# Performance work log

Measured on AMD Instinct MI355X. Metric: run time of the kernel, lower is better.

The kernel has to match this reference:

```python
import jax, jax.numpy as jnp
import numpy as np

HEAD_N = 16
EMBED_D = 1024
MASK_FILL = 1e-09  # source uses masked_fill(mask==0, 1e-09), NOT -inf


def setup_inputs() -> dict:
    key = jax.random.key(0)
    ks = jax.random.split(key, 8)
    B, S, D = 4, 4096, EMBED_D
    L = S // HEAD_N
    q = jax.random.normal(ks[0], (B, S, D), dtype=jnp.float32)
    k = jax.random.normal(ks[1], (B, S, D), dtype=jnp.float32)
    v = jax.random.normal(ks[2], (B, S, D), dtype=jnp.float32)
    mask = jax.random.randint(ks[3], (B, L, L), 0, 2, dtype=jnp.int32)
    scale = 0.02
    Wq = jax.random.normal(ks[4], (D, D), dtype=jnp.float32) * scale
    Wk = jax.random.normal(ks[5], (D, D), dtype=jnp.float32) * scale
    Wv = jax.random.normal(ks[6], (D, D), dtype=jnp.float32) * scale
    Wo = jax.random.normal(ks[7], (D, D), dtype=jnp.float32) * scale
    return {"q": q, "k": k, "v": v, "mask": mask, "Wq": Wq, "Wk": Wk, "Wv": Wv, "Wo": Wo}


def _split_heads(x, B):
    # Faithful to source bug: view(B, -1, head_n, embedding_d).transpose(1, 2)
    # -> splits the SEQUENCE dim by head_n; per-head dim stays EMBED_D.
    return x.reshape(B, -1, HEAD_N, EMBED_D).transpose(0, 2, 1, 3)  # [B,h,L,D]


def reference(q, k, v, mask, Wq, Wk, Wv, Wo):
    B, S, D = q.shape
    qh = _split_heads(q @ Wq, B)
    kh = _split_heads(k @ Wk, B)
    vh = _split_heads(v @ Wv, B)
    # score: [B, h, L, L], L = S // head_n
    score = jnp.einsum("bhld,bhmd->bhlm", qh, kh) / jnp.sqrt(jnp.float32(D))
    m = mask[:, None, :, :]  # unsqueeze(1) -> broadcast over heads
    score = jnp.where(m == 0, jnp.float32(MASK_FILL), score)
    att = jax.nn.softmax(score, axis=-1)  # dropout p=0.0 -> identity
    x = jnp.einsum("bhlm,bhmd->bhld", att, vh)  # [B,h,L,D]
    x = x.transpose(0, 2, 1, 3).reshape(B, S, D)
    return x @ Wo
```

## Files before the change

kernel.cpp:

```cpp
#include <hip/hip_runtime.h>
#include <hip/hip_bf16.h>

typedef __bf16 bf16x8 __attribute__((ext_vector_type(8)));
typedef float f32x4 __attribute__((ext_vector_type(4)));
typedef unsigned short ushort_t;
typedef unsigned int uint_t;

#define HN 16
#define LSEQ 256
#define DD 1024
#define BB 4
#define SS 4096
#define MROWS (BB * SS)
#define BHN (BB * HN)

__device__ __forceinline__ ushort_t f2bf(float f) {
  uint_t u = __builtin_bit_cast(uint_t, f);
  u += 0x7fffu + ((u >> 16) & 1u);
  return (ushort_t)(u >> 16);
}
__device__ __forceinline__ uint_t pk2(float lo, float hi) {
  return (uint_t)f2bf(lo) | ((uint_t)f2bf(hi) << 16);
}

__global__ __launch_bounds__(256) void cvt_bf16(const float4* __restrict__ in,
                                                uint4* __restrict__ out) {
  const long i = (long)blockIdx.x * 256 + threadIdx.x;
  const float4 a = in[i * 2];
  const float4 b = in[i * 2 + 1];
  uint4 o;
  o.x = pk2(a.x, a.y);
  o.y = pk2(a.z, a.w);
  o.z = pk2(b.x, b.y);
  o.w = pk2(b.z, b.w);
  out[i] = o;
}

__global__ __launch_bounds__(256) void transpose_w(const float* __restrict__ W,
                                                   ushort_t* __restrict__ WT) {
  __shared__ float tile[32][33];
  const int tx = threadIdx.x, ty = threadIdx.y;
  const int bn = blockIdx.x * 32, bk = blockIdx.y * 32;
#pragma unroll
  for (int j = 0; j < 32; j += 8)
    tile[ty + j][tx] = W[(long)(bk + ty + j) * DD + bn + tx];
  __syncthreads();
#pragma unroll
  for (int j = 0; j < 32; j += 8)
    WT[(long)(bn + ty + j) * DD + bk + tx] = f2bf(tile[tx][ty + j]);
}

__global__ __launch_bounds__(256) void transpose_v(const ushort_t* __restrict__ vh,
                                                   ushort_t* __restrict__ vhT) {
  __shared__ ushort_t tile[32][33];
  const int tx = threadIdx.x, ty = threadIdx.y;
  const long zo = (long)blockIdx.z * (LSEQ * DD);
  const ushort_t* src = vh + zo;
  ushort_t* dst = vhT + zo;
  const int bd = blockIdx.x * 32;
  const int bl = blockIdx.y * 32;
#pragma unroll
  for (int j = 0; j < 32; j += 8)
    tile[ty + j][tx] = src[(long)(bl + ty + j) * DD + bd + tx];
  __syncthreads();
#pragma unroll
  for (int j = 0; j < 32; j += 8)
    dst[(long)(bd + ty + j) * LSEQ + bl + tx] = tile[tx][ty + j];
}

__global__ __launch_bounds__(256) void softmax_mask(const float* __restrict__ Sc,
                                                    const int* __restrict__ mask,
                                                    ushort_t* __restrict__ att) {
  const int wid = threadIdx.x >> 6, lane = threadIdx.x & 63;
  const int g = blockIdx.x * 4 + wid;
  const int bh = g >> 8, l = g & 255;
  const int b = bh >> 4;
  const float4 sv = *(const float4*)&Sc[(long)g * 256 + lane * 4];
  const int4 mv = *(const int4*)&mask[((long)b * 256 + l) * 256 + lane * 4];
  float s[4];
  s[0] = (mv.x == 0) ? 1e-9f : sv.x * 0.03125f;
  s[1] = (mv.y == 0) ? 1e-9f : sv.y * 0.03125f;
  s[2] = (mv.z == 0) ? 1e-9f : sv.z * 0.03125f;
  s[3] = (mv.w == 0) ? 1e-9f : sv.w * 0.03125f;
  float mx = fmaxf(fmaxf(s[0], s[1]), fmaxf(s[2], s[3]));
#pragma unroll
  for (int off = 32; off; off >>= 1) mx = fmaxf(mx, __shfl_xor(mx, off));
  float e[4], sum = 0.f;
#pragma unroll
  for (int i = 0; i < 4; ++i) {
    e[i] = __expf(s[i] - mx);
    sum += e[i];
  }
#pragma unroll
  for (int off = 32; off; off >>= 1) sum += __shfl_xor(sum, off);
  const float inv = 1.0f / sum;
  ushort4 o;
  o.x = f2bf(e[0] * inv);
  o.y = f2bf(e[1] * inv);
  o.z = f2bf(e[2] * inv);
  o.w = f2bf(e[3] * inv);
  *(ushort4*)&att[(long)g * 256 + lane * 4] = o;
}

template <int SMODE>
__global__ __launch_bounds__(256, 2) void gemm_tn(const ushort_t* __restrict__ Ab,
                                                  const ushort_t* __restrict__ Btp,
                                                  void* __restrict__ Cp, int K, int ldA,
                                                  int ldB, int ldC, long batchA,
                                                  long batchB, long batchC) {
  __shared__ ushort_t smem[16384];
  ushort_t* sA = smem;
  ushort_t* sB = smem + 8192;

  const int bx = blockIdx.x, by = blockIdx.y, z = blockIdx.z;
  const int rowBase = by * 128;
  const int colBase = bx * 128;

  const int t = threadIdx.x;
  const int lane = t & 63;
  const int wid = t >> 6;
  const int wr = (wid >> 1) * 64;
  const int wc = (wid & 1) * 64;
  const int fr = lane & 15;
  const int fk = (lane >> 4) * 8;

  const ushort_t* Atile = Ab + batchA * z + (long)rowBase * ldA;
  const ushort_t* Btile = Btp + batchB * z + (long)colBase * ldB;

  f32x4 acc[4][4];
#pragma unroll
  for (int m = 0; m < 4; ++m)
#pragma unroll
    for (int n = 0; n < 4; ++n) acc[m][n] = (f32x4){0.f, 0.f, 0.f, 0.f};

  const int NT = K >> 5;

  auto stageAB = [&](int buf, int kt) {
    const long ko = (long)kt * 32;
#pragma unroll
    for (int i = 0; i < 2; ++i) {
      const int c = i * 256 + t;
      const int cw = i * 256 + (t & 192);
      __builtin_amdgcn_global_load_lds(
          (const __attribute__((address_space(1))) void*)(Atile + (long)(c >> 2) * ldA + ko +
                                                          (c & 3) * 8),
          (__attribute__((address_space(3))) void*)(sA + buf * 4096 + cw * 8), 16, 0, 0);
      __builtin_amdgcn_global_load_lds(
          (const __attribute__((address_space(1))) void*)(Btile + (long)(c >> 2) * ldB + ko +
                                                          (c & 3) * 8),
          (__attribute__((address_space(3))) void*)(sB + buf * 4096 + cw * 8), 16, 0, 0);
    }
  };

  stageAB(0, 0);
  __syncthreads();

  int cur = 0;
  for (int kt = 0; kt < NT; ++kt) {
    if (kt + 1 < NT) stageAB(cur ^ 1, kt + 1);

    bf16x8 af[4], bfv[4];
    const ushort_t* baseA = sA + cur * 4096 + fk;
    const ushort_t* baseB = sB + cur * 4096 + fk;
#pragma unroll
    for (int m = 0; m < 4; ++m) af[m] = *(const bf16x8*)(baseA + (wr + m * 16 + fr) * 32);
#pragma unroll
    for (int n = 0; n < 4; ++n) bfv[n] = *(const bf16x8*)(baseB + (wc + n * 16 + fr) * 32);

#pragma unroll
    for (int m = 0; m < 4; ++m)
#pragma unroll
      for (int n = 0; n < 4; ++n)
        acc[m][n] = __builtin_amdgcn_mfma_f32_16x16x32_bf16(af[m], bfv[n], acc[m][n], 0, 0, 0);

    __syncthreads();
    cur ^= 1;
  }

  const int rq = (lane >> 4) * 4;
  if constexpr (SMODE == 0) {
    float* Cf = (float*)Cp + batchC * z;
#pragma unroll
    for (int m = 0; m < 4; ++m)
#pragma unroll
      for (int n = 0; n < 4; ++n)
#pragma unroll
        for (int r = 0; r < 4; ++r)
          Cf[(long)(rowBase + wr + m * 16 + rq + r) * ldC + colBase + wc + n * 16 + fr] =
              acc[m][n][r];
  } else {
#pragma unroll
    for (int m = 0; m < 4; ++m)
#pragma unroll
      for (int n = 0; n < 4; ++n)
#pragma unroll
        for (int r = 0; r < 4; ++r)
          smem[(wr + m * 16 + rq + r) * 128 + wc + n * 16 + fr] = f2bf(acc[m][n][r]);
    __syncthreads();
    ushort_t* Cb = (ushort_t*)Cp;
    const int c8 = (lane & 15) * 8;
#pragma unroll
    for (int i = 0; i < 8; ++i) {
      const int row = i * 16 + wid * 4 + (lane >> 4);
      const uint4 val = *(const uint4*)(smem + row * 128 + c8);
      const int l = rowBase + row;
      const int orow = ((z >> 4) << 12) + l * 16 + (z & 15);
      *(uint4*)(Cb + (long)orow * 1024 + colBase + c8) = val;
    }
  }
}

#define SBAR() asm volatile("s_barrier" ::: "memory")
#define LGKM0() asm volatile("s_waitcnt lgkmcnt(0)" ::: "memory")
#define VMW2() asm volatile("s_waitcnt vmcnt(2)" ::: "memory")
#define VMW0() asm volatile("s_waitcnt vmcnt(0)" ::: "memory")

template <int SMODE>
__global__ __launch_bounds__(512, 1) void gemm256(const ushort_t* __restrict__ Ab,
                                                  const ushort_t* __restrict__ Btp,
                                                  void* __restrict__ Cp, int K, int ldA,
                                                  int ldB, int ldC, int nbx) {
  __shared__ ushort_t sm[65536];

  const int orig = blockIdx.x;
  const int cpx = (int)gridDim.x >> 3;
  const int wgid = (orig & 7) * cpx + (orig >> 3);
  const int by = wgid / nbx, bx = wgid % nbx;
  const int rowBase = by * 256, colBase = bx * 256;

  const int t = threadIdx.x;
  const int lane = t & 63;
  const int wid = t >> 6;
  const int wm = wid >> 2;
  const int wn = wid & 3;
  const int fr = lane & 15;
  const int q = lane >> 4;

  const int sw0 = ((q ^ (fr & 7)) * 8);
  const int sw1 = (((4 + q) ^ (fr & 7)) * 8);
  const int aoff0 = fr * 64 + sw0;
  const int aoff1 = fr * 64 + sw1;
  const int bbase = ((wn & 1) * 64 + fr) * 64;
  const int boff0 = bbase + sw0;
  const int boff1 = bbase + sw1;

  const ushort_t* srcA[2][2];
  const ushort_t* srcB[2][2];
  int ldsoff[2];
#pragma unroll
  for (int i = 0; i < 2; ++i) {
    const int c = i * 512 + t;
    const int rowc = c >> 3;
    const int gc = (c & 7) ^ (rowc & 7);
    srcA[0][i] = Ab + (long)(rowBase + rowc) * ldA + gc * 8;
    srcA[1][i] = Ab + (long)(rowBase + 128 + rowc) * ldA + gc * 8;
    srcB[0][i] = Btp + (long)(colBase + rowc) * ldB + gc * 8;
    srcB[1][i] = Btp + (long)(colBase + 128 + rowc) * ldB + gc * 8;
    ldsoff[i] = (c & ~63) * 8;
  }

#define STAGE(kind, h, T)                                                                   \
  do {                                                                                      \
    ushort_t* _d = sm + ((kind) ? 32768 : 0) + ((T) & 1) * 16384 + (h) * 8192;              \
    const ushort_t* _s0 = ((kind) ? srcB[h][0] : srcA[h][0]) + (long)(T) * 64;              \
    __builtin_amdgcn_global_load_lds((const __attribute__((address_space(1))) void*)_s0,    \
                                     (__attribute__((address_space(3))) void*)(_d + ldsoff[0]), \
                                     16, 0, 0);                                             \
    const ushort_t* _s1 = ((kind) ? srcB[h][1] : srcA[h][1]) + (long)(T) * 64;              \
    __builtin_amdgcn_global_load_lds((const __attribute__((address_space(1))) void*)_s1,    \
                                     (__attribute__((address_space(3))) void*)(_d + ldsoff[1]), \
                                     16, 0, 0);                                             \
  } while (0)

  f32x4 acc[8][4];
#pragma unroll
  for (int m = 0; m < 8; ++m)
#pragma unroll
    for (int n = 0; n < 4; ++n) acc[m][n] = (f32x4){0.f, 0.f, 0.f, 0.f};

  bf16x8 af[4][2], bf0[2][2], bf1[2][2];

#define LDA4(dbuf, msub)                                                         \
  do {                                                                           \
    const ushort_t* _b = sm + (dbuf)*16384 + wm * 8192 + (msub)*4096;            \
    _Pragma("unroll") for (int m2 = 0; m2 < 4; ++m2) {                           \
      af[m2][0] = *(const bf16x8*)(_b + m2 * 1024 + aoff0);                      \
      af[m2][1] = *(const bf16x8*)(_b + m2 * 1024 + aoff1);                      \
    }                                                                            \
  } while (0)

#define LDB2(dbuf, nsub, bfv)                                                    \
  do {                                                                           \
    const ushort_t* _b = sm + 32768 + (dbuf)*16384 + (wn >> 1) * 8192 + (nsub)*2048; \
    _Pragma("unroll") for (int n2 = 0; n2 < 2; ++n2) {                           \
      bfv[n2][0] = *(const bf16x8*)(_b + n2 * 1024 + boff0);                     \
      bfv[n2][1] = *(const bf16x8*)(_b + n2 * 1024 + boff1);                     \
    }                                                                            \
  } while (0)

#define MMQ(msub, nsub, bfv)                                                     \
  do {                                                                           \
    _Pragma("unroll") for (int m2 = 0; m2 < 4; ++m2)                             \
        _Pragma("unroll") for (int n2 = 0; n2 < 2; ++n2) {                       \
      acc[(msub)*4 + m2][(nsub)*2 + n2] = __builtin_amdgcn_mfma_f32_16x16x32_bf16( \
          af[m2][0], bfv[n2][0], acc[(msub)*4 + m2][(nsub)*2 + n2], 0, 0, 0);    \
      acc[(msub)*4 + m2][(nsub)*2 + n2] = __builtin_amdgcn_mfma_f32_16x16x32_bf16( \
          af[m2][1], bfv[n2][1], acc[(msub)*4 + m2][(nsub)*2 + n2], 0, 0, 0);    \
    }                                                                            \
  } while (0)

#define PH_OPEN() SBAR(); LGKM0(); __builtin_amdgcn_s_setprio(1)
#define PH_CLOSE() __builtin_amdgcn_s_setprio(0); SBAR()

  const int NT = K >> 6;
  const int NI = NT >> 1;

  STAGE(0, 0, 0);
  STAGE(0, 1, 0);
  STAGE(1, 0, 0);
  STAGE(1, 1, 0);
  STAGE(0, 0, 1);
  VMW2();
  SBAR();

  for (int it = 0; it < NI - 1; ++it) {
    const int T0 = 2 * it;
    LDA4(0, 0);
    LDB2(0, 0, bf0);
    STAGE(0, 1, T0 + 1);
    PH_OPEN(); MMQ(0, 0, bf0); PH_CLOSE();
    LDB2(0, 1, bf1);
    STAGE(1, 0, T0 + 1);
    PH_OPEN(); MMQ(0, 1, bf1); PH_CLOSE();
    LDA4(0, 1);
    STAGE(1, 1, T0 + 1);
    PH_OPEN(); MMQ(1, 1, bf1); PH_CLOSE();
    STAGE(0, 0, T0 + 2);
    SBAR();
    __builtin_amdgcn_s_setprio(1);
    MMQ(1, 0, bf0);
    __builtin_amdgcn_s_setprio(0);
    VMW2();
    SBAR();
    LDA4(1, 0);
    LDB2(1, 0, bf0);
    STAGE(0, 1, T0 + 2);
    PH_OPEN(); MMQ(0, 0, bf0); PH_CLOSE();
    LDB2(1, 1, bf1);
    STAGE(1, 0, T0 + 2);
    PH_OPEN(); MMQ(0, 1, bf1); PH_CLOSE();
    LDA4(1, 1);
    STAGE(1, 1, T0 + 2);
    PH_OPEN(); MMQ(1, 1, bf1); PH_CLOSE();
    STAGE(0, 0, T0 + 3);
    SBAR();
    __builtin_amdgcn_s_setprio(1);
    MMQ(1, 0, bf0);
    __builtin_amdgcn_s_setprio(0);
    VMW2();
    SBAR();
  }

  {
    LDA4(0, 0);
    LDB2(0, 0, bf0);
    STAGE(0, 1, NT - 1);
    PH_OPEN(); MMQ(0, 0, bf0); PH_CLOSE();
    LDB2(0, 1, bf1);
    STAGE(1, 0, NT - 1);
    PH_OPEN(); MMQ(0, 1, bf1); PH_CLOSE();
    LDA4(0, 1);
    STAGE(1, 1, NT - 1);
    PH_OPEN(); MMQ(1, 1, bf1); PH_CLOSE();
    SBAR();
    __builtin_amdgcn_s_setprio(1);
    MMQ(1, 0, bf0);
    __builtin_amdgcn_s_setprio(0);
    VMW0();
    SBAR();
    LDA4(1, 0);
    LDB2(1, 0, bf0);
    PH_OPEN(); MMQ(0, 0, bf0); PH_CLOSE();
    LDB2(1, 1, bf1);
    PH_OPEN(); MMQ(0, 1, bf1); PH_CLOSE();
    LDA4(1, 1);
    PH_OPEN(); MMQ(1, 1, bf1); PH_CLOSE();
    SBAR();
    MMQ(1, 0, bf0);
    SBAR();
  }

  const int rq = q * 4;
  if constexpr (SMODE == 0) {
    float* Cf = (float*)Cp;
#pragma unroll
    for (int m = 0; m < 8; ++m)
#pragma unroll
      for (int n = 0; n < 4; ++n)
#pragma unroll
        for (int r = 0; r < 4; ++r) {
          const int row = rowBase + wm * 128 + m * 16 + rq + r;
          const int col = colBase + wn * 64 + n * 16 + fr;
          Cf[(long)row * ldC + col] = acc[m][n][r];
        }
  } else {
#pragma unroll
    for (int m = 0; m < 8; ++m)
#pragma unroll
      for (int n = 0; n < 4; ++n)
#pragma unroll
        for (int r = 0; r < 4; ++r) {
          const int row = wm * 128 + m * 16 + rq + r;
          const int col = wn * 64 + n * 16 + fr;
          sm[row * 256 + (((col >> 3) ^ (row & 7)) * 8) + (col & 7)] = f2bf(acc[m][n][r]);
        }
    __syncthreads();
    ushort_t* Cb = (ushort_t*)Cp;
    const int cc = t & 31;
    const int r0 = t >> 5;
#pragma unroll
    for (int i = 0; i < 16; ++i) {
      const int row = r0 + i * 16;
      const uint4 val = *(const uint4*)(sm + row * 256 + ((cc ^ (row & 7)) * 8));
      const int grow = rowBase + row;
      const int b = grow >> 12;
      const int s = grow & 4095;
      const int orow = ((b << 4) + (s & 15)) * 256 + (s >> 4);
      *(uint4*)(Cb + (long)orow * 1024 + colBase + cc * 8) = val;
    }
  }
#undef STAGE
#undef LDA4
#undef LDB2
#undef MMQ
#undef PH_OPEN
#undef PH_CLOSE
}

extern "C" void kernel_launch(void* const* d_in, const int* in_sizes, int n_in,
                              void* d_out, int out_size, void* d_ws, size_t ws_size,
                              hipStream_t stream) {
  const float* q = (const float*)d_in[0];
  const float* k = (const float*)d_in[1];
  const float* v = (const float*)d_in[2];
  const int* mask = (const int*)d_in[3];
  const float* Wq = (const float*)d_in[4];
  const float* Wk = (const float*)d_in[5];
  const float* Wv = (const float*)d_in[6];
  const float* Wo = (const float*)d_in[7];
  float* out = (float*)d_out;

  char* ws = (char*)d_ws;
  const size_t MB = 1024 * 1024;
  ushort_t* WTq = (ushort_t*)(ws + 0 * MB);
  ushort_t* WTk = (ushort_t*)(ws + 2 * MB);
  ushort_t* WTv = (ushort_t*)(ws + 4 * MB);
  ushort_t* WTo = (ushort_t*)(ws + 6 * MB);
  ushort_t* buf0 = (ushort_t*)(ws + 8 * MB);
  ushort_t* qh = (ushort_t*)(ws + 40 * MB);
  ushort_t* kh = (ushort_t*)(ws + 72 * MB);
  ushort_t* vh = (ushort_t*)(ws + 104 * MB);
  ushort_t* vhT = (ushort_t*)(ws + 136 * MB);
  float* Sc = (float*)buf0;
  ushort_t* att = qh;
  ushort_t* x = kh;

  const dim3 tb(32, 8);
  transpose_w<<<dim3(32, 32), tb, 0, stream>>>(Wq, WTq);
  transpose_w<<<dim3(32, 32), tb, 0, stream>>>(Wk, WTk);
  transpose_w<<<dim3(32, 32), tb, 0, stream>>>(Wv, WTv);
  transpose_w<<<dim3(32, 32), tb, 0, stream>>>(Wo, WTo);

  cvt_bf16<<<8192, 256, 0, stream>>>((const float4*)q, (uint4*)buf0);
  gemm256<1><<<256, 512, 0, stream>>>(buf0, WTq, qh, 1024, 1024, 1024, 1024, 4);
  cvt_bf16<<<8192, 256, 0, stream>>>((const float4*)k, (uint4*)buf0);
  gemm256<1><<<256, 512, 0, stream>>>(buf0, WTk, kh, 1024, 1024, 1024, 1024, 4);
  cvt_bf16<<<8192, 256, 0, stream>>>((const float4*)v, (uint4*)buf0);
  gemm256<1><<<256, 512, 0, stream>>>(buf0, WTv, vh, 1024, 1024, 1024, 1024, 4);

  transpose_v<<<dim3(32, 8, BHN), tb, 0, stream>>>(vh, vhT);

  gemm_tn<0><<<dim3(2, 2, BHN), 256, 0, stream>>>(qh, kh, Sc, 1024, 1024, 1024, 256,
                                                  (long)256 * 1024, (long)256 * 1024,
                                                  (long)65536);
  softmax_mask<<<4096, 256, 0, stream>>>(Sc, mask, att);

  gemm_tn<2><<<dim3(8, 2, BHN), 256, 0, stream>>>(att, vhT, x, 256, 256, 256, 1024,
                                                  (long)65536, (long)262144, 0);

  gemm256<0><<<256, 512, 0, stream>>>(x, WTo, out, 1024, 1024, 1024, 1024, 4);
}
```

Before: 292.1 us.

## Fuse QK^T scores with masked softmax and batch QKV projections into one launch

Adds a score_sm kernel that computes the Q·K^T tile for 64 query rows in LDS, then applies the mask and softmax in place. This removes the fp32 score round-trip through global memory and the separate softmax launch. When the workspace is large enough, the three input conversions and three projection GEMMs are also merged into one launch each, over a z dimension, which should give better occupancy (768 blocks). The four weight transposes are merged into one launch too. The fused score kernel uses 80KB of LDS and only 256 blocks, which may cost occupancy.

```diff
diff --git a/kernel.cpp b/kernel.cpp
--- a/kernel.cpp
+++ b/kernel.cpp
@@ -23,8 +23,12 @@
   return (uint_t)f2bf(lo) | ((uint_t)f2bf(hi) << 16);
 }
 
-__global__ __launch_bounds__(256) void cvt_bf16(const float4* __restrict__ in,
-                                                uint4* __restrict__ out) {
+__global__ __launch_bounds__(256) void cvt3(const float4* __restrict__ s0,
+                                            const float4* __restrict__ s1,
+                                            const float4* __restrict__ s2,
+                                            uint4* __restrict__ out) {
+  const int z = blockIdx.y;
+  const float4* in = (z == 0) ? s0 : (z == 1) ? s1 : s2;
   const long i = (long)blockIdx.x * 256 + threadIdx.x;
   const float4 a = in[i * 2];
   const float4 b = in[i * 2 + 1];
@@ -33,12 +37,18 @@
   o.y = pk2(a.z, a.w);
   o.z = pk2(b.x, b.y);
   o.w = pk2(b.z, b.w);
-  out[i] = o;
-}
-
-__global__ __launch_bounds__(256) void transpose_w(const float* __restrict__ W,
-                                                   ushort_t* __restrict__ WT) {
+  out[(long)z * 2097152 + i] = o;
+}
+
+__global__ __launch_bounds__(256) void transpose_w4(const float* __restrict__ W0,
+                                                    const float* __restrict__ W1,
+                                                    const float* __restrict__ W2,
+                                                    const float* __restrict__ W3,
+                                                    ushort_t* __restrict__ WT) {
   __shared__ float tile[32][33];
+  const int z = blockIdx.z;
+  const float* W = (z == 0) ? W0 : (z == 1) ? W1 : (z == 2) ? W2 : W3;
+  ushort_t* dst = WT + (long)z * 1048576;
   const int tx = threadIdx.x, ty = threadIdx.y;
   const int bn = blockIdx.x * 32, bk = blockIdx.y * 32;
 #pragma unroll
@@ -47,7 +57,7 @@
   __syncthreads();
 #pragma unroll
   for (int j = 0; j < 32; j += 8)
-    WT[(long)(bn + ty + j) * DD + bk + tx] = f2bf(tile[tx][ty + j]);
+    dst[(long)(bn + ty + j) * DD + bk + tx] = f2bf(tile[tx][ty + j]);
 }
 
 __global__ __launch_bounds__(256) void transpose_v(const ushort_t* __restrict__ vh,
@@ -68,38 +78,130 @@
     dst[(long)(bd + ty + j) * LSEQ + bl + tx] = tile[tx][ty + j];
 }
 
-__global__ __launch_bounds__(256) void softmax_mask(const float* __restrict__ Sc,
-                                                    const int* __restrict__ mask,
-                                                    ushort_t* __restrict__ att) {
-  const int wid = threadIdx.x >> 6, lane = threadIdx.x & 63;
-  const int g = blockIdx.x * 4 + wid;
-  const int bh = g >> 8, l = g & 255;
+__global__ __launch_bounds__(256, 2) void score_sm(const ushort_t* __restrict__ qh,
+                                                   const ushort_t* __restrict__ kh,
+                                                   const int* __restrict__ mask,
+                                                   ushort_t* __restrict__ att) {
+  __shared__ char smemraw[81920];
+  ushort_t* sA = (ushort_t*)smemraw;
+  ushort_t* sB = (ushort_t*)(smemraw + 16384);
+  float* Sf = (float*)smemraw;
+
+  const int orig = blockIdx.x;
+  const int wgid = (orig & 7) * 32 + (orig >> 3);
+  const int bh = wgid >> 2, rb = wgid & 3;
   const int b = bh >> 4;
-  const float4 sv = *(const float4*)&Sc[(long)g * 256 + lane * 4];
-  const int4 mv = *(const int4*)&mask[((long)b * 256 + l) * 256 + lane * 4];
-  float s[4];
-  s[0] = (mv.x == 0) ? 1e-9f : sv.x * 0.03125f;
-  s[1] = (mv.y == 0) ? 1e-9f : sv.y * 0.03125f;
-  s[2] = (mv.z == 0) ? 1e-9f : sv.z * 0.03125f;
-  s[3] = (mv.w == 0) ? 1e-9f : sv.w * 0.03125f;
-  float mx = fmaxf(fmaxf(s[0], s[1]), fmaxf(s[2], s[3]));
-#pragma unroll
-  for (int off = 32; off; off >>= 1) mx = fmaxf(mx, __shfl_xor(mx, off));
-  float e[4], sum = 0.f;
-#pragma unroll
-  for (int i = 0; i < 4; ++i) {
-    e[i] = __expf(s[i] - mx);
-    sum += e[i];
-  }
-#pragma unroll
-  for (int off = 32; off; off >>= 1) sum += __shfl_xor(sum, off);
-  const float inv = 1.0f / sum;
-  ushort4 o;
-  o.x = f2bf(e[0] * inv);
-  o.y = f2bf(e[1] * inv);
-  o.z = f2bf(e[2] * inv);
-  o.w = f2bf(e[3] * inv);
-  *(ushort4*)&att[(long)g * 256 + lane * 4] = o;
+  const ushort_t* A = qh + ((long)bh * 256 + rb * 64) * 1024;
+  const ushort_t* Bk = kh + (long)bh * 256 * 1024;
+
+  const int t = threadIdx.x, lane = t & 63, wid = t >> 6;
+  const int fr = lane & 15, q = lane >> 4;
+  const int wc = wid * 64;
+  const int sw0 = (q ^ (fr & 7)) * 8;
+  const int sw1 = ((4 + q) ^ (fr & 7)) * 8;
+
+  int srcAo[2], dstA[2], srcBo[8], dstB[8];
+#pragma unroll
+  for (int i = 0; i < 2; ++i) {
+    const int c = i * 256 + t, row = c >> 3, gc = (c & 7) ^ (row & 7);
+    srcAo[i] = row * 1024 + gc * 8;
+    dstA[i] = (i * 256 + (t & 192)) * 8;
+  }
+#pragma unroll
+  for (int i = 0; i < 8; ++i) {
+    const int c = i * 256 + t, row = c >> 3, gc = (c & 7) ^ (row & 7);
+    srcBo[i] = row * 1024 + gc * 8;
+    dstB[i] = (i * 256 + (t & 192)) * 8;
+  }
+
+  auto stage = [&](int buf, int kt) {
+    const int ko = kt * 64;
+#pragma unroll
+    for (int i = 0; i < 2; ++i)
+      __builtin_amdgcn_global_load_lds(
+          (const __attribute__((address_space(1))) void*)(A + srcAo[i] + ko),
+          (__attribute__((address_space(3))) void*)(sA + buf * 4096 + dstA[i]), 16, 0, 0);
+#pragma unroll
+    for (int i = 0; i < 8; ++i)
+      __builtin_amdgcn_global_load_lds(
+          (const __attribute__((address_space(1))) void*)(Bk + srcBo[i] + ko),
+          (__attribute__((address_space(3))) void*)(sB + buf * 16384 + dstB[i]), 16, 0, 0);
+  };
+
+  f32x4 acc[4][4];
+#pragma unroll
+  for (int m = 0; m < 4; ++m)
+#pragma unroll
+    for (int n = 0; n < 4; ++n) acc[m][n] = (f32x4){0.f, 0.f, 0.f, 0.f};
+
+  stage(0, 0);
+  __syncthreads();
+  int cur = 0;
+  for (int kt = 0; kt < 16; ++kt) {
+    if (kt < 15) stage(cur ^ 1, kt + 1);
+    bf16x8 af[4][2], bfv[4][2];
+    const ushort_t* bA = sA + cur * 4096;
+    const ushort_t* bB = sB + cur * 16384;
+#pragma unroll
+    for (int m = 0; m < 4; ++m) {
+      af[m][0] = *(const bf16x8*)(bA + (m * 16 + fr) * 64 + sw0);
+      af[m][1] = *(const bf16x8*)(bA + (m * 16 + fr) * 64 + sw1);
+    }
+#pragma unroll
+    for (int n = 0; n < 4; ++n) {
+      bfv[n][0] = *(const bf16x8*)(bB + (wc + n * 16 + fr) * 64 + sw0);
+      bfv[n][1] = *(const bf16x8*)(bB + (wc + n * 16 + fr) * 64 + sw1);
+    }
+#pragma unroll
+    for (int m = 0; m < 4; ++m)
+#pragma unroll
+      for (int n = 0; n < 4; ++n) {
+        acc[m][n] = __builtin_amdgcn_mfma_f32_16x16x32_bf16(af[m][0], bfv[n][0], acc[m][n], 0, 0, 0);
+        acc[m][n] = __builtin_amdgcn_mfma_f32_16x16x32_bf16(af[m][1], bfv[n][1], acc[m][n], 0, 0, 0);
+      }
+    __syncthreads();
+    cur ^= 1;
+  }
+
+#pragma unroll
+  for (int m = 0; m < 4; ++m)
+#pragma unroll
+    for (int n = 0; n < 4; ++n)
+#pragma unroll
+      for (int r = 0; r < 4; ++r)
+        Sf[(m * 16 + q * 4 + r) * 256 + wc + n * 16 + fr] = acc[m][n][r];
+  __syncthreads();
+
+#pragma unroll 2
+  for (int i = 0; i < 16; ++i) {
+    const int row = wid * 16 + i;
+    const int gl = rb * 64 + row;
+    const f32x4 sv = *(const f32x4*)&Sf[row * 256 + lane * 4];
+    const int4 mv = *(const int4*)&mask[((long)b * 256 + gl) * 256 + lane * 4];
+    float s[4];
+    s[0] = (mv.x == 0) ? 1e-9f : sv[0] * 0.03125f;
+    s[1] = (mv.y == 0) ? 1e-9f : sv[1] * 0.03125f;
+    s[2] = (mv.z == 0) ? 1e-9f : sv[2] * 0.03125f;
+    s[3] = (mv.w == 0) ? 1e-9f : sv[3] * 0.03125f;
+    float mx = fmaxf(fmaxf(s[0], s[1]), fmaxf(s[2], s[3]));
+#pragma unroll
+    for (int off = 32; off; off >>= 1) mx = fmaxf(mx, __shfl_xor(mx, off));
+    float e[4], sum = 0.f;
+#pragma unroll
+    for (int j = 0; j < 4; ++j) {
+      e[j] = __expf(s[j] - mx);
+      sum += e[j];
+    }
+#pragma unroll
+    for (int off = 32; off; off >>= 1) sum += __shfl_xor(sum, off);
+    const float inv = 1.0f / sum;
+    ushort4 o;
+    o.x = f2bf(e[0] * inv);
+    o.y = f2bf(e[1] * inv);
+    o.z = f2bf(e[2] * inv);
+    o.w = f2bf(e[3] * inv);
+    *(ushort4*)&att[((long)bh * 256 + gl) * 256 + lane * 4] = o;
+  }
 }
 
 template <int SMODE>
@@ -178,17 +280,7 @@
   }
 
   const int rq = (lane >> 4) * 4;
-  if constexpr (SMODE == 0) {
-    float* Cf = (float*)Cp + batchC * z;
-#pragma unroll
-    for (int m = 0; m < 4; ++m)
-#pragma unroll
-      for (int n = 0; n < 4; ++n)
-#pragma unroll
-        for (int r = 0; r < 4; ++r)
-          Cf[(long)(rowBase + wr + m * 16 + rq + r) * ldC + colBase + wc + n * 16 + fr] =
-              acc[m][n][r];
-  } else {
+  {
 #pragma unroll
     for (int m = 0; m < 4; ++m)
 #pragma unroll
@@ -216,17 +308,24 @@
 #define VMW0() asm volatile("s_waitcnt vmcnt(0)" ::: "memory")
 
 template <int SMODE>
-__global__ __launch_bounds__(512, 1) void gemm256(const ushort_t* __restrict__ Ab,
+__global__ __launch_bounds__(512, 1) void gemm256(const ushort_t* __restrict__ A0,
+                                                  const ushort_t* __restrict__ A1,
+                                                  const ushort_t* __restrict__ A2,
                                                   const ushort_t* __restrict__ Btp,
-                                                  void* __restrict__ Cp, int K, int ldA,
-                                                  int ldB, int ldC, int nbx) {
+                                                  void* __restrict__ Cp, long bStrideZ,
+                                                  long cStrideZ) {
   __shared__ ushort_t sm[65536];
 
   const int orig = blockIdx.x;
   const int cpx = (int)gridDim.x >> 3;
   const int wgid = (orig & 7) * cpx + (orig >> 3);
-  const int by = wgid / nbx, bx = wgid % nbx;
+  const int z = wgid >> 8;
+  const int tile = wgid & 255;
+  const int by = tile >> 2, bx = tile & 3;
   const int rowBase = by * 256, colBase = bx * 256;
+
+  const ushort_t* Ab = (z == 0) ? A0 : (z == 1) ? A1 : A2;
+  const ushort_t* Bt = Btp + bStrideZ * z;
 
   const int t = threadIdx.x;
   const int lane = t & 63;
@@ -252,10 +351,10 @@
     const int c = i * 512 + t;
     const int rowc = c >> 3;
     const int gc = (c & 7) ^ (rowc & 7);
-    srcA[0][i] = Ab + (long)(rowBase + rowc) * ldA + gc * 8;
-    srcA[1][i] = Ab + (long)(rowBase + 128 + rowc) * ldA + gc * 8;
-    srcB[0][i] = Btp + (long)(colBase + rowc) * ldB + gc * 8;
-    srcB[1][i] = Btp + (long)(colBase + 128 + rowc) * ldB + gc * 8;
+    srcA[0][i] = Ab + (long)(rowBase + rowc) * 1024 + gc * 8;
+    srcA[1][i] = Ab + (long)(rowBase + 128 + rowc) * 1024 + gc * 8;
+    srcB[0][i] = Bt + (long)(colBase + rowc) * 1024 + gc * 8;
+    srcB[1][i] = Bt + (long)(colBase + 128 + rowc) * 1024 + gc * 8;
     ldsoff[i] = (c & ~63) * 8;
   }
 
@@ -312,8 +411,8 @@
 #define PH_OPEN() SBAR(); LGKM0(); __builtin_amdgcn_s_setprio(1)
 #define PH_CLOSE() __builtin_amdgcn_s_setprio(0); SBAR()
 
-  const int NT = K >> 6;
-  const int NI = NT >> 1;
+  const int NT = 16;
+  const int NI = 8;
 
   STAGE(0, 0, 0);
   STAGE(0, 1, 0);
@@ -392,7 +491,7 @@
 
   const int rq = q * 4;
   if constexpr (SMODE == 0) {
-    float* Cf = (float*)Cp;
+    float* Cf = (float*)Cp + cStrideZ * z;
 #pragma unroll
     for (int m = 0; m < 8; ++m)
 #pragma unroll
@@ -401,7 +500,7 @@
         for (int r = 0; r < 4; ++r) {
           const int row = rowBase + wm * 128 + m * 16 + rq + r;
           const int col = colBase + wn * 64 + n * 16 + fr;
-          Cf[(long)row * ldC + col] = acc[m][n][r];
+          Cf[(long)row * 1024 + col] = acc[m][n][r];
         }
   } else {
 #pragma unroll
@@ -415,7 +514,7 @@
           sm[row * 256 + (((col >> 3) ^ (row & 7)) * 8) + (col & 7)] = f2bf(acc[m][n][r]);
         }
     __syncthreads();
-    ushort_t* Cb = (ushort_t*)Cp;
+    ushort_t* Cb = (ushort_t*)Cp + cStrideZ * z;
     const int cc = t & 31;
     const int r0 = t >> 5;
 #pragma unroll
@@ -452,41 +551,53 @@
 
   char* ws = (char*)d_ws;
   const size_t MB = 1024 * 1024;
-  ushort_t* WTq = (ushort_t*)(ws + 0 * MB);
-  ushort_t* WTk = (ushort_t*)(ws + 2 * MB);
-  ushort_t* WTv = (ushort_t*)(ws + 4 * MB);
-  ushort_t* WTo = (ushort_t*)(ws + 6 * MB);
-  ushort_t* buf0 = (ushort_t*)(ws + 8 * MB);
-  ushort_t* qh = (ushort_t*)(ws + 40 * MB);
-  ushort_t* kh = (ushort_t*)(ws + 72 * MB);
-  ushort_t* vh = (ushort_t*)(ws + 104 * MB);
-  ushort_t* vhT = (ushort_t*)(ws + 136 * MB);
-  float* Sc = (float*)buf0;
-  ushort_t* att = qh;
-  ushort_t* x = kh;
-
+  ushort_t* WT = (ushort_t*)ws;
   const dim3 tb(32, 8);
-  transpose_w<<<dim3(32, 32), tb, 0, stream>>>(Wq, WTq);
-  transpose_w<<<dim3(32, 32), tb, 0, stream>>>(Wk, WTk);
-  transpose_w<<<dim3(32, 32), tb, 0, stream>>>(Wv, WTv);
-  transpose_w<<<dim3(32, 32), tb, 0, stream>>>(Wo, WTo);
-
-  cvt_bf16<<<8192, 256, 0, stream>>>((const float4*)q, (uint4*)buf0);
-  gemm256<1><<<256, 512, 0, stream>>>(buf0, WTq, qh, 1024, 1024, 1024, 1024, 4);
-  cvt_bf16<<<8192, 256, 0, stream>>>((const float4*)k, (uint4*)buf0);
-  gemm256<1><<<256, 512, 0, stream>>>(buf0, WTk, kh, 1024, 1024, 1024, 1024, 4);
-  cvt_bf16<<<8192, 256, 0, stream>>>((const float4*)v, (uint4*)buf0);
-  gemm256<1><<<256, 512, 0, stream>>>(buf0, WTv, vh, 1024, 1024, 1024, 1024, 4);
-
-  transpose_v<<<dim3(32, 8, BHN), tb, 0, stream>>>(vh, vhT);
-
-  gemm_tn<0><<<dim3(2, 2, BHN), 256, 0, stream>>>(qh, kh, Sc, 1024, 1024, 1024, 256,
-                                                  (long)256 * 1024, (long)256 * 1024,
-                                                  (long)65536);
-  softmax_mask<<<4096, 256, 0, stream>>>(Sc, mask, att);
-
-  gemm_tn<2><<<dim3(8, 2, BHN), 256, 0, stream>>>(att, vhT, x, 256, 256, 256, 1024,
-                                                  (long)65536, (long)262144, 0);
-
-  gemm256<0><<<256, 512, 0, stream>>>(x, WTo, out, 1024, 1024, 1024, 1024, 4);
-}
+  transpose_w4<<<dim3(32, 32, 4), tb, 0, stream>>>(Wq, Wk, Wv, Wo, WT);
+
+  const bool big = ws_size >= (size_t)200 * MB;
+
+  if (big) {
+    ushort_t* qkvb = (ushort_t*)(ws + 8 * MB);
+    ushort_t* qh = (ushort_t*)(ws + 104 * MB);
+    ushort_t* kh = (ushort_t*)(ws + 136 * MB);
+    ushort_t* vh = (ushort_t*)(ws + 168 * MB);
+    ushort_t* vhT = (ushort_t*)(ws + 8 * MB);
+    ushort_t* att = (ushort_t*)(ws + 40 * MB);
+    ushort_t* x = (ushort_t*)(ws + 48 * MB);
+
+    cvt3<<<dim3(8192, 3), 256, 0, stream>>>((const float4*)q, (const float4*)k,
+                                            (const float4*)v, (uint4*)qkvb);
+    gemm256<1><<<768, 512, 0, stream>>>(qkvb, qkvb + (size_t)16777216,
+                                        qkvb + (size_t)33554432, WT, qh, 1 << 20,
+                                        (long)16777216);
+    transpose_v<<<dim3(32, 8, BHN), tb, 0, stream>>>(vh, vhT);
+    score_sm<<<256, 256, 0, stream>>>(qh, kh, mask, att);
+    gemm_tn<2><<<dim3(8, 2, BHN), 256, 0, stream>>>(att, vhT, x, 256, 256, 256, 1024,
+                                                    (long)65536, (long)262144, 0);
+    gemm256<0><<<256, 512, 0, stream>>>(x, x, x, WT + (size_t)3145728, out, 0, 0);
+  } else {
+    ushort_t* qb = (ushort_t*)(ws + 8 * MB);
+    ushort_t* qh = (ushort_t*)(ws + 40 * MB);
+    ushort_t* kh = (ushort_t*)(ws + 72 * MB);
+    ushort_t* vh = (ushort_t*)(ws + 104 * MB);
+    ushort_t* vhT = (ushort_t*)(ws + 136 * MB);
+    ushort_t* att = (ushort_t*)(ws + 8 * MB);
+    ushort_t* x = (ushort_t*)(ws + 16 * MB);
+
+    cvt3<<<dim3(8192, 1), 256, 0, stream>>>((const float4*)q, (const float4*)q,
+                                            (const float4*)q, (uint4*)qb);
+    gemm256<1><<<256, 512, 0, stream>>>(qb, qb, qb, WT, qh, 0, 0);
+    cvt3<<<dim3(8192, 1), 256, 0, stream>>>((const float4*)k, (const float4*)k,
+                                            (const float4*)k, (uint4*)qb);
+    gemm256<1><<<256, 512, 0, stream>>>(qb, qb, qb, WT + (size_t)1048576, kh, 0, 0);
+    cvt3<<<dim3(8192, 1), 256, 0, stream>>>((const float4*)v, (const float4*)v,
+                                            (const float4*)v, (uint4*)qb);
+    gemm256<1><<<256, 512, 0, stream>>>(qb, qb, qb, WT + (size_t)2097152, vh, 0, 0);
+    transpose_v<<<dim3(32, 8, BHN), tb, 0, stream>>>(vh, vhT);
+    score_sm<<<256, 256, 0, stream>>>(qh, kh, mask, att);
+    gemm_tn<2><<<dim3(8, 2, BHN), 256, 0, stream>>>(att, vhT, x, 256, 256, 256, 1024,
+                                                    (long)65536, (long)262144, 0);
+    gemm256<0><<<256, 512, 0, stream>>>(x, x, x, WT + (size_t)3145728, out, 0, 0);
+  }
+}
```

New measurement: 270.5 us. -7.4%, faster.
